# Kernel optimization log

Measured on AMD Instinct MI355X. Metric: run time of the kernel, lower is better.

Reference implementation:

```python
import jax, jax.numpy as jnp
import numpy as np

N_NODES = 100000
N_EDGES = 1600000
D = 64


def setup_inputs() -> dict:
    key = jax.random.key(0)
    k1, k2, k3, k4 = jax.random.split(key, 4)
    x = jax.random.normal(k1, (N_NODES, D), dtype=jnp.float32)
    src = jax.random.randint(k2, (N_EDGES,), 0, N_NODES, dtype=jnp.int64)
    dst = jax.random.randint(k3, (N_EDGES,), 0, N_NODES, dtype=jnp.int64)
    W = jax.random.normal(k4, (D, D), dtype=jnp.float32) / np.sqrt(D)
    b = jnp.zeros((D,), dtype=jnp.float32)
    return {"x": x, "src": src, "dst": dst, "W": W, "b": b}


def reference(x, src, dst, W, b):
    # DGL GraphConv, norm='both': h = D_in^{-1/2} A D_out^{-1/2} x W + b
    n = x.shape[0]
    ones = jnp.ones(src.shape[0], dtype=x.dtype)
    deg_out = jax.ops.segment_sum(ones, src, num_segments=n)  # out-degree of sources
    deg_in = jax.ops.segment_sum(ones, dst, num_segments=n)   # in-degree of dests
    norm_src = jnp.maximum(deg_out, 1.0) ** -0.5              # DGL clamps degs to >=1
    norm_dst = jnp.maximum(deg_in, 1.0) ** -0.5
    x_n = x * norm_src[:, None]                               # [N, D]
    agg = jax.ops.segment_sum(x_n[src], dst, num_segments=n)  # SpMM: [N, D]
    h = agg * norm_dst[:, None]
    # linear transform + bias; activation=None, dropout=0.0 (identity)
    return h @ W + b
```

## Files before the change

kernel.cpp:

```cpp
#include <hip/hip_runtime.h>
#include <hip/hip_bf16.h>

#define ND 64

#define DBKT_W 64
#define LOG_DBKT 6
#define NDBKT_MAX 1600
#define DCAP 1280

#define SBKT_W 256
#define LOG_SBKT 8
#define NSBKT_MAX 400
#define SCAP 4608

#define PART_EDGES 6400
#define COL_CAP DCAP

typedef __attribute__((ext_vector_type(8))) short bf16x8;
typedef __attribute__((ext_vector_type(4))) float f32x4;

__device__ __forceinline__ unsigned bf16rn(float f) {
    unsigned u = __float_as_uint(f);
    return (u + 0x7fffu + ((u >> 16) & 1u)) >> 16;
}
__device__ __forceinline__ unsigned pack2(float lo, float hi) {
    return bf16rn(lo) | (bf16rn(hi) << 16);
}

__global__ __launch_bounds__(256) void part_kernel(
        const int* __restrict__ src, const int* __restrict__ dst,
        int* __restrict__ cnt_d, int* __restrict__ cnt_s,
        int* __restrict__ ebuf, unsigned char* __restrict__ ebuf2,
        int E, int nbkt_d, int nbkt_s) {
    __shared__ int hbd[NDBKT_MAX], hcd[NDBKT_MAX];
    __shared__ int hbs[NSBKT_MAX], hcs[NSBKT_MAX];
    const int base_e = blockIdx.x * PART_EDGES;
    const int nE = min(PART_EDGES, E - base_e);
    for (int i = threadIdx.x; i < nbkt_d; i += blockDim.x) { hbd[i] = 0; hcd[i] = 0; }
    for (int i = threadIdx.x; i < nbkt_s; i += blockDim.x) { hbs[i] = 0; hcs[i] = 0; }
    __syncthreads();
    const int nq = nE >> 2;
    for (int i = threadIdx.x; i < nq; i += blockDim.x) {
        int4 s = ((const int4*)(src + base_e))[i];
        int4 d = ((const int4*)(dst + base_e))[i];
        atomicAdd(&hbd[d.x >> LOG_DBKT], 1); atomicAdd(&hbd[d.y >> LOG_DBKT], 1);
        atomicAdd(&hbd[d.z >> LOG_DBKT], 1); atomicAdd(&hbd[d.w >> LOG_DBKT], 1);
        atomicAdd(&hbs[s.x >> LOG_SBKT], 1); atomicAdd(&hbs[s.y >> LOG_SBKT], 1);
        atomicAdd(&hbs[s.z >> LOG_SBKT], 1); atomicAdd(&hbs[s.w >> LOG_SBKT], 1);
    }
    for (int e = (nq << 2) + threadIdx.x; e < nE; e += blockDim.x) {
        atomicAdd(&hbd[dst[base_e + e] >> LOG_DBKT], 1);
        atomicAdd(&hbs[src[base_e + e] >> LOG_SBKT], 1);
    }
    __syncthreads();
    for (int i = threadIdx.x; i < nbkt_d; i += blockDim.x) {
        int c = hbd[i];
        hbd[i] = c ? (i * DCAP + atomicAdd(&cnt_d[i], c)) : 0;
    }
    for (int i = threadIdx.x; i < nbkt_s; i += blockDim.x) {
        int c = hbs[i];
        hbs[i] = c ? (i * SCAP + atomicAdd(&cnt_s[i], c)) : 0;
    }
    __syncthreads();
    for (int i = threadIdx.x; i < nq; i += blockDim.x) {
        int4 s = ((const int4*)(src + base_e))[i];
        int4 d = ((const int4*)(dst + base_e))[i];
        int b0 = d.x >> LOG_DBKT, b1 = d.y >> LOG_DBKT;
        int b2 = d.z >> LOG_DBKT, b3 = d.w >> LOG_DBKT;
        int p0 = hbd[b0] + atomicAdd(&hcd[b0], 1);
        int p1 = hbd[b1] + atomicAdd(&hcd[b1], 1);
        int p2 = hbd[b2] + atomicAdd(&hcd[b2], 1);
        int p3 = hbd[b3] + atomicAdd(&hcd[b3], 1);
        if (p0 < (b0 + 1) * DCAP) ebuf[p0] = (s.x << LOG_DBKT) | (d.x & (DBKT_W - 1));
        if (p1 < (b1 + 1) * DCAP) ebuf[p1] = (s.y << LOG_DBKT) | (d.y & (DBKT_W - 1));
        if (p2 < (b2 + 1) * DCAP) ebuf[p2] = (s.z << LOG_DBKT) | (d.z & (DBKT_W - 1));
        if (p3 < (b3 + 1) * DCAP) ebuf[p3] = (s.w << LOG_DBKT) | (d.w & (DBKT_W - 1));
        int c0 = s.x >> LOG_SBKT, c1 = s.y >> LOG_SBKT;
        int c2 = s.z >> LOG_SBKT, c3 = s.w >> LOG_SBKT;
        int q0 = hbs[c0] + atomicAdd(&hcs[c0], 1);
        int q1 = hbs[c1] + atomicAdd(&hcs[c1], 1);
        int q2 = hbs[c2] + atomicAdd(&hcs[c2], 1);
        int q3 = hbs[c3] + atomicAdd(&hcs[c3], 1);
        if (q0 < (c0 + 1) * SCAP) ebuf2[q0] = (unsigned char)(s.x & (SBKT_W - 1));
        if (q1 < (c1 + 1) * SCAP) ebuf2[q1] = (unsigned char)(s.y & (SBKT_W - 1));
        if (q2 < (c2 + 1) * SCAP) ebuf2[q2] = (unsigned char)(s.z & (SBKT_W - 1));
        if (q3 < (c3 + 1) * SCAP) ebuf2[q3] = (unsigned char)(s.w & (SBKT_W - 1));
    }
    for (int e = (nq << 2) + threadIdx.x; e < nE; e += blockDim.x) {
        int s = src[base_e + e], d = dst[base_e + e];
        int bk = d >> LOG_DBKT;
        int p = hbd[bk] + atomicAdd(&hcd[bk], 1);
        if (p < (bk + 1) * DCAP) ebuf[p] = (s << LOG_DBKT) | (d & (DBKT_W - 1));
        int ck = s >> LOG_SBKT;
        int q = hbs[ck] + atomicAdd(&hcs[ck], 1);
        if (q < (ck + 1) * SCAP) ebuf2[q] = (unsigned char)(s & (SBKT_W - 1));
    }
}

__global__ __launch_bounds__(256) void yprep_kernel(
        const float4* __restrict__ x4,
        const unsigned char* __restrict__ ebuf2,
        const int* __restrict__ cnt_s,
        uint4* __restrict__ y4,
        const float* __restrict__ W, unsigned* __restrict__ wpk, int n) {
    __shared__ int cnt[SBKT_W];
    const int bkt = blockIdx.x;
    const int node0 = bkt << LOG_SBKT;
    if (threadIdx.x < SBKT_W) cnt[threadIdx.x] = 0;
    if (bkt == 0) {
        for (int i = threadIdx.x; i < 2048; i += blockDim.x) {
            int l = i >> 5, d = i & 31;
            int colb = l & 15, kb = (l >> 4) * 8;
            int t = d >> 3, s = (d >> 2) & 1, m = d & 3;
            float lo = W[(32 * s + kb + 2 * m) * ND + 16 * t + colb];
            float hi = W[(32 * s + kb + 2 * m + 1) * ND + 16 * t + colb];
            wpk[i] = pack2(lo, hi);
        }
    }
    __syncthreads();
    const int beg = bkt * SCAP;
    const int end = beg + min(cnt_s[bkt], SCAP);
    for (int i = beg + (int)threadIdx.x; i < end; i += blockDim.x)
        atomicAdd(&cnt[ebuf2[i]], 1);
    __syncthreads();
#pragma unroll
    for (int it = 0; it < 8; ++it) {
        int item = it * 256 + threadIdx.x;
        int row = item >> 3, q = item & 7;
        int grow = node0 + row;
        if (grow >= n) continue;
        float nr = rsqrtf(fmaxf((float)cnt[row], 1.0f));
        float4 a = x4[(size_t)grow * 16 + q * 2];
        float4 b = x4[(size_t)grow * 16 + q * 2 + 1];
        uint4 o;
        o.x = pack2(a.x * nr, a.y * nr);
        o.y = pack2(a.z * nr, a.w * nr);
        o.z = pack2(b.x * nr, b.y * nr);
        o.w = pack2(b.z * nr, b.w * nr);
        y4[(size_t)grow * 8 + q] = o;
    }
}

__global__ __launch_bounds__(256) void spmm_kernel(
        const unsigned* __restrict__ y32,
        const int* __restrict__ ebuf,
        const int* __restrict__ cnt_d,
        const unsigned* __restrict__ wpk,
        const float* __restrict__ bias,
        float* __restrict__ out, int n, int nbkt) {
    __shared__ int colS[COL_CAP];
    __shared__ int rp[DBKT_W + 1];
    __shared__ int cur[DBKT_W];
    __shared__ int degl[DBKT_W];
    __shared__ unsigned hS[4][16 * 32];

    const int lane = threadIdx.x & 63;
    const int q    = lane >> 4;
    const int f    = lane & 15;
    const int g    = threadIdx.x >> 6;
    const int colb = lane & 15;
    const uint2* Y2 = (const uint2*)y32;

    bf16x8 bw[4][2];
#pragma unroll
    for (int t = 0; t < 4; ++t)
#pragma unroll
        for (int s = 0; s < 2; ++s)
            bw[t][s] = *(const bf16x8*)&wpk[lane * 32 + (t * 2 + s) * 4];
    float bb[4];
#pragma unroll
    for (int t = 0; t < 4; ++t) bb[t] = bias[16 * t + colb];

    for (int bkt = blockIdx.x; bkt < nbkt; bkt += gridDim.x) {
        const int ebeg = bkt * DCAP;
        const int ne   = min(cnt_d[bkt], DCAP);
        const int node0 = bkt << LOG_DBKT;
        const int nn = min(DBKT_W, n - node0);

        if (threadIdx.x < DBKT_W) degl[threadIdx.x] = 0;
        __syncthreads();
        for (int i = threadIdx.x; i < ne; i += blockDim.x)
            atomicAdd(&degl[ebuf[ebeg + i] & (DBKT_W - 1)], 1);
        __syncthreads();
        if (g == 0) {
            int v = degl[lane];
            int sv = v;
#pragma unroll
            for (int off = 1; off < 64; off <<= 1) {
                int t = __shfl_up(sv, off, 64);
                if (lane >= off) sv += t;
            }
            int ex = sv - v;
            rp[lane] = ex;
            cur[lane] = ex;
            if (lane == 63) rp[DBKT_W] = sv;
        }
        __syncthreads();
        for (int i = threadIdx.x; i < ne; i += blockDim.x) {
            int p = ebuf[ebeg + i];
            int pos = atomicAdd(&cur[p & (DBKT_W - 1)], 1);
            if (pos < COL_CAP) colS[pos] = p >> LOG_DBKT;
        }
        __syncthreads();

#pragma unroll 1
        for (int it = 0; it < 4; ++it) {
            const int ln = (g << 4) + (it << 2) + q;
            const bool act = ln < nn;
            const int beg = act ? rp[ln] : 0;
            const int end = act ? rp[ln + 1] : 0;
            float A0 = 0.f, A1 = 0.f, A2 = 0.f, A3 = 0.f;
            float B0 = 0.f, B1 = 0.f, B2 = 0.f, B3 = 0.f;
            int j = beg;
            for (; j + 8 <= end; j += 8) {
                int e0 = colS[j],     e1 = colS[j + 1];
                int e2 = colS[j + 2], e3 = colS[j + 3];
                int e4 = colS[j + 4], e5 = colS[j + 5];
                int e6 = colS[j + 6], e7 = colS[j + 7];
                uint2 u0 = Y2[(size_t)e0 * 16 + f];
                uint2 u1 = Y2[(size_t)e1 * 16 + f];
                uint2 u2 = Y2[(size_t)e2 * 16 + f];
                uint2 u3 = Y2[(size_t)e3 * 16 + f];
                uint2 u4 = Y2[(size_t)e4 * 16 + f];
                uint2 u5 = Y2[(size_t)e5 * 16 + f];
                uint2 u6 = Y2[(size_t)e6 * 16 + f];
                uint2 u7 = Y2[(size_t)e7 * 16 + f];
                A0 += __uint_as_float(u0.x << 16); A1 += __uint_as_float(u0.x & 0xffff0000u);
                A2 += __uint_as_float(u0.y << 16); A3 += __uint_as_float(u0.y & 0xffff0000u);
                B0 += __uint_as_float(u1.x << 16); B1 += __uint_as_float(u1.x & 0xffff0000u);
                B2 += __uint_as_float(u1.y << 16); B3 += __uint_as_float(u1.y & 0xffff0000u);
                A0 += __uint_as_float(u2.x << 16); A1 += __uint_as_float(u2.x & 0xffff0000u);
                A2 += __uint_as_float(u2.y << 16); A3 += __uint_as_float(u2.y & 0xffff0000u);
                B0 += __uint_as_float(u3.x << 16); B1 += __uint_as_float(u3.x & 0xffff0000u);
                B2 += __uint_as_float(u3.y << 16); B3 += __uint_as_float(u3.y & 0xffff0000u);
                A0 += __uint_as_float(u4.x << 16); A1 += __uint_as_float(u4.x & 0xffff0000u);
                A2 += __uint_as_float(u4.y << 16); A3 += __uint_as_float(u4.y & 0xffff0000u);
                B0 += __uint_as_float(u5.x << 16); B1 += __uint_as_float(u5.x & 0xffff0000u);
                B2 += __uint_as_float(u5.y << 16); B3 += __uint_as_float(u5.y & 0xffff0000u);
                A0 += __uint_as_float(u6.x << 16); A1 += __uint_as_float(u6.x & 0xffff0000u);
                A2 += __uint_as_float(u6.y << 16); A3 += __uint_as_float(u6.y & 0xffff0000u);
                B0 += __uint_as_float(u7.x << 16); B1 += __uint_as_float(u7.x & 0xffff0000u);
                B2 += __uint_as_float(u7.y << 16); B3 += __uint_as_float(u7.y & 0xffff0000u);
            }
            for (; j + 2 <= end; j += 2) {
                int e0 = colS[j], e1 = colS[j + 1];
                uint2 u0 = Y2[(size_t)e0 * 16 + f];
                uint2 u1 = Y2[(size_t)e1 * 16 + f];
                A0 += __uint_as_float(u0.x << 16); A1 += __uint_as_float(u0.x & 0xffff0000u);
                A2 += __uint_as_float(u0.y << 16); A3 += __uint_as_float(u0.y & 0xffff0000u);
                B0 += __uint_as_float(u1.x << 16); B1 += __uint_as_float(u1.x & 0xffff0000u);
                B2 += __uint_as_float(u1.y << 16); B3 += __uint_as_float(u1.y & 0xffff0000u);
            }
            if (j < end) {
                int e0 = colS[j];
                uint2 u0 = Y2[(size_t)e0 * 16 + f];
                A0 += __uint_as_float(u0.x << 16); A1 += __uint_as_float(u0.x & 0xffff0000u);
                A2 += __uint_as_float(u0.y << 16); A3 += __uint_as_float(u0.y & 0xffff0000u);
            }
            if (act) {
                float nd = rsqrtf(fmaxf((float)(end - beg), 1.0f));
                uint2 wv;
                wv.x = pack2((A0 + B0) * nd, (A1 + B1) * nd);
                wv.y = pack2((A2 + B2) * nd, (A3 + B3) * nd);
                *(uint2*)&hS[g][(((it << 2) + q) << 5) + (f << 1)] = wv;
            }
        }
        __syncthreads();

        if ((g << 4) < nn) {
            const unsigned* hrow = &hS[g][colb * 32 + ((lane >> 4) << 2)];
            bf16x8 a0 = *(const bf16x8*)hrow;
            bf16x8 a1 = *(const bf16x8*)(hrow + 16);
#pragma unroll
            for (int t = 0; t < 4; ++t) {
                f32x4 z = {0.f, 0.f, 0.f, 0.f};
                z = __builtin_amdgcn_mfma_f32_16x16x32_bf16(a0, bw[t][0], z, 0, 0, 0);
                z = __builtin_amdgcn_mfma_f32_16x16x32_bf16(a1, bw[t][1], z, 0, 0, 0);
#pragma unroll
                for (int r = 0; r < 4; ++r) {
                    int rowD = ((lane >> 4) << 2) + r;
                    int li = (g << 4) + rowD;
                    if (li < nn)
                        out[(size_t)(node0 + li) * ND + 16 * t + colb] = z[r] + bb[t];
                }
            }
        }
        __syncthreads();
    }
}

extern "C" void kernel_launch(void* const* d_in, const int* in_sizes, int n_in,
                              void* d_out, int out_size, void* d_ws, size_t ws_size,
                              hipStream_t stream) {
    const float* x   = (const float*)d_in[0];
    const int*   src = (const int*)d_in[1];
    const int*   dst = (const int*)d_in[2];
    const float* W   = (const float*)d_in[3];
    const float* b   = (const float*)d_in[4];
    float*       out = (float*)d_out;

    const int n = in_sizes[0] / ND;
    const int E = in_sizes[1];
    const int nbkt_d = (n + DBKT_W - 1) / DBKT_W;
    const int nbkt_s = (n + SBKT_W - 1) / SBKT_W;

    char* ws = (char*)d_ws;
    unsigned* y32   = (unsigned*)ws;
    int*      ebuf  = (int*)(y32 + (size_t)n * 32);
    int*      cnt_d = ebuf + (size_t)NDBKT_MAX * DCAP;
    int*      cnt_s = cnt_d + NDBKT_MAX;
    unsigned* wpk   = (unsigned*)(cnt_s + NSBKT_MAX);
    unsigned char* ebuf2 = (unsigned char*)(wpk + 2048);

    hipMemsetAsync(cnt_d, 0, (size_t)(NDBKT_MAX + NSBKT_MAX) * sizeof(int), stream);

    part_kernel<<<(E + PART_EDGES - 1) / PART_EDGES, 256, 0, stream>>>(
        src, dst, cnt_d, cnt_s, ebuf, ebuf2, E, nbkt_d, nbkt_s);
    yprep_kernel<<<nbkt_s, 256, 0, stream>>>(
        (const float4*)x, ebuf2, cnt_s, (uint4*)y32, W, wpk, n);
    spmm_kernel<<<nbkt_d, 256, 0, stream>>>(y32, ebuf, cnt_d, wpk, b, out, n, nbkt_d);
}
```

Before: 99.57 us.

## Widen SpMM gathers to 16-byte rows, shrink partition blocks, register-cache edges

The partition kernel now takes 2048 edges per block. Each thread holds its 8 edges in registers, and the base offsets are bumped in place, which removes the second counter arrays and the second global read. The degree-count kernel reads the byte bucket 16 bytes at a time. The SpMM kernel caches bucket edges in registers between the degree pass and the scatter pass. It also gathers 16-byte rows with 8 lanes per node instead of 8-byte rows with 16 lanes, so more nodes are in flight per wave at the cost of more registers. The fast partition path relies on the 2048-edge block size exactly matching 2 int4 loads per thread.

Measured after the change: 118.5 us. 1.19x slower.

```diff
diff --git a/kernel.cpp b/kernel.cpp
--- a/kernel.cpp
+++ b/kernel.cpp
@@ -13,7 +13,7 @@
 #define NSBKT_MAX 400
 #define SCAP 4608
 
-#define PART_EDGES 6400
+#define PART_EDGES 2048
 #define COL_CAP DCAP
 
 typedef __attribute__((ext_vector_type(8))) short bf16x8;
@@ -32,68 +32,76 @@
         int* __restrict__ cnt_d, int* __restrict__ cnt_s,
         int* __restrict__ ebuf, unsigned char* __restrict__ ebuf2,
         int E, int nbkt_d, int nbkt_s) {
-    __shared__ int hbd[NDBKT_MAX], hcd[NDBKT_MAX];
-    __shared__ int hbs[NSBKT_MAX], hcs[NSBKT_MAX];
+    __shared__ int hbd[NDBKT_MAX];
+    __shared__ int hbs[NSBKT_MAX];
     const int base_e = blockIdx.x * PART_EDGES;
     const int nE = min(PART_EDGES, E - base_e);
-    for (int i = threadIdx.x; i < nbkt_d; i += blockDim.x) { hbd[i] = 0; hcd[i] = 0; }
-    for (int i = threadIdx.x; i < nbkt_s; i += blockDim.x) { hbs[i] = 0; hcs[i] = 0; }
+    for (int i = threadIdx.x; i < nbkt_d; i += blockDim.x) hbd[i] = 0;
+    for (int i = threadIdx.x; i < nbkt_s; i += blockDim.x) hbs[i] = 0;
     __syncthreads();
-    const int nq = nE >> 2;
-    for (int i = threadIdx.x; i < nq; i += blockDim.x) {
-        int4 s = ((const int4*)(src + base_e))[i];
-        int4 d = ((const int4*)(dst + base_e))[i];
-        atomicAdd(&hbd[d.x >> LOG_DBKT], 1); atomicAdd(&hbd[d.y >> LOG_DBKT], 1);
-        atomicAdd(&hbd[d.z >> LOG_DBKT], 1); atomicAdd(&hbd[d.w >> LOG_DBKT], 1);
-        atomicAdd(&hbs[s.x >> LOG_SBKT], 1); atomicAdd(&hbs[s.y >> LOG_SBKT], 1);
-        atomicAdd(&hbs[s.z >> LOG_SBKT], 1); atomicAdd(&hbs[s.w >> LOG_SBKT], 1);
-    }
-    for (int e = (nq << 2) + threadIdx.x; e < nE; e += blockDim.x) {
-        atomicAdd(&hbd[dst[base_e + e] >> LOG_DBKT], 1);
-        atomicAdd(&hbs[src[base_e + e] >> LOG_SBKT], 1);
-    }
-    __syncthreads();
-    for (int i = threadIdx.x; i < nbkt_d; i += blockDim.x) {
-        int c = hbd[i];
-        hbd[i] = c ? (i * DCAP + atomicAdd(&cnt_d[i], c)) : 0;
-    }
-    for (int i = threadIdx.x; i < nbkt_s; i += blockDim.x) {
-        int c = hbs[i];
-        hbs[i] = c ? (i * SCAP + atomicAdd(&cnt_s[i], c)) : 0;
-    }
-    __syncthreads();
-    for (int i = threadIdx.x; i < nq; i += blockDim.x) {
-        int4 s = ((const int4*)(src + base_e))[i];
-        int4 d = ((const int4*)(dst + base_e))[i];
-        int b0 = d.x >> LOG_DBKT, b1 = d.y >> LOG_DBKT;
-        int b2 = d.z >> LOG_DBKT, b3 = d.w >> LOG_DBKT;
-        int p0 = hbd[b0] + atomicAdd(&hcd[b0], 1);
-        int p1 = hbd[b1] + atomicAdd(&hcd[b1], 1);
-        int p2 = hbd[b2] + atomicAdd(&hcd[b2], 1);
-        int p3 = hbd[b3] + atomicAdd(&hcd[b3], 1);
-        if (p0 < (b0 + 1) * DCAP) ebuf[p0] = (s.x << LOG_DBKT) | (d.x & (DBKT_W - 1));
-        if (p1 < (b1 + 1) * DCAP) ebuf[p1] = (s.y << LOG_DBKT) | (d.y & (DBKT_W - 1));
-        if (p2 < (b2 + 1) * DCAP) ebuf[p2] = (s.z << LOG_DBKT) | (d.z & (DBKT_W - 1));
-        if (p3 < (b3 + 1) * DCAP) ebuf[p3] = (s.w << LOG_DBKT) | (d.w & (DBKT_W - 1));
-        int c0 = s.x >> LOG_SBKT, c1 = s.y >> LOG_SBKT;
-        int c2 = s.z >> LOG_SBKT, c3 = s.w >> LOG_SBKT;
-        int q0 = hbs[c0] + atomicAdd(&hcs[c0], 1);
-        int q1 = hbs[c1] + atomicAdd(&hcs[c1], 1);
-        int q2 = hbs[c2] + atomicAdd(&hcs[c2], 1);
-        int q3 = hbs[c3] + atomicAdd(&hcs[c3], 1);
-        if (q0 < (c0 + 1) * SCAP) ebuf2[q0] = (unsigned char)(s.x & (SBKT_W - 1));
-        if (q1 < (c1 + 1) * SCAP) ebuf2[q1] = (unsigned char)(s.y & (SBKT_W - 1));
-        if (q2 < (c2 + 1) * SCAP) ebuf2[q2] = (unsigned char)(s.z & (SBKT_W - 1));
-        if (q3 < (c3 + 1) * SCAP) ebuf2[q3] = (unsigned char)(s.w & (SBKT_W - 1));
-    }
-    for (int e = (nq << 2) + threadIdx.x; e < nE; e += blockDim.x) {
-        int s = src[base_e + e], d = dst[base_e + e];
-        int bk = d >> LOG_DBKT;
-        int p = hbd[bk] + atomicAdd(&hcd[bk], 1);
-        if (p < (bk + 1) * DCAP) ebuf[p] = (s << LOG_DBKT) | (d & (DBKT_W - 1));
-        int ck = s >> LOG_SBKT;
-        int q = hbs[ck] + atomicAdd(&hcs[ck], 1);
-        if (q < (ck + 1) * SCAP) ebuf2[q] = (unsigned char)(s & (SBKT_W - 1));
+
+    if (nE == PART_EDGES) {
+        const int4* s4 = (const int4*)(src + base_e);
+        const int4* d4 = (const int4*)(dst + base_e);
+        int4 s0 = s4[threadIdx.x], s1 = s4[256 + threadIdx.x];
+        int4 d0 = d4[threadIdx.x], d1 = d4[256 + threadIdx.x];
+        atomicAdd(&hbd[d0.x >> LOG_DBKT], 1); atomicAdd(&hbd[d0.y >> LOG_DBKT], 1);
+        atomicAdd(&hbd[d0.z >> LOG_DBKT], 1); atomicAdd(&hbd[d0.w >> LOG_DBKT], 1);
+        atomicAdd(&hbd[d1.x >> LOG_DBKT], 1); atomicAdd(&hbd[d1.y >> LOG_DBKT], 1);
+        atomicAdd(&hbd[d1.z >> LOG_DBKT], 1); atomicAdd(&hbd[d1.w >> LOG_DBKT], 1);
+        atomicAdd(&hbs[s0.x >> LOG_SBKT], 1); atomicAdd(&hbs[s0.y >> LOG_SBKT], 1);
+        atomicAdd(&hbs[s0.z >> LOG_SBKT], 1); atomicAdd(&hbs[s0.w >> LOG_SBKT], 1);
+        atomicAdd(&hbs[s1.x >> LOG_SBKT], 1); atomicAdd(&hbs[s1.y >> LOG_SBKT], 1);
+        atomicAdd(&hbs[s1.z >> LOG_SBKT], 1); atomicAdd(&hbs[s1.w >> LOG_SBKT], 1);
+        __syncthreads();
+        for (int i = threadIdx.x; i < nbkt_d; i += blockDim.x) {
+            int c = hbd[i];
+            hbd[i] = c ? (i * DCAP + atomicAdd(&cnt_d[i], c)) : 0;
+        }
+        for (int i = threadIdx.x; i < nbkt_s; i += blockDim.x) {
+            int c = hbs[i];
+            hbs[i] = c ? (i * SCAP + atomicAdd(&cnt_s[i], c)) : 0;
+        }
+        __syncthreads();
+        {
+            int sv[8] = {s0.x, s0.y, s0.z, s0.w, s1.x, s1.y, s1.z, s1.w};
+            int dv[8] = {d0.x, d0.y, d0.z, d0.w, d1.x, d1.y, d1.z, d1.w};
+#pragma unroll
+            for (int k = 0; k < 8; ++k) {
+                int b = dv[k] >> LOG_DBKT;
+                int p = atomicAdd(&hbd[b], 1);
+                if (p < (b + 1) * DCAP)
+                    ebuf[p] = (sv[k] << LOG_DBKT) | (dv[k] & (DBKT_W - 1));
+                int c = sv[k] >> LOG_SBKT;
+                int q = atomicAdd(&hbs[c], 1);
+                if (q < (c + 1) * SCAP)
+                    ebuf2[q] = (unsigned char)(sv[k] & (SBKT_W - 1));
+            }
+        }
+    } else {
+        for (int e = (int)threadIdx.x; e < nE; e += blockDim.x) {
+            atomicAdd(&hbd[dst[base_e + e] >> LOG_DBKT], 1);
+            atomicAdd(&hbs[src[base_e + e] >> LOG_SBKT], 1);
+        }
+        __syncthreads();
+        for (int i = threadIdx.x; i < nbkt_d; i += blockDim.x) {
+            int c = hbd[i];
+            hbd[i] = c ? (i * DCAP + atomicAdd(&cnt_d[i], c)) : 0;
+        }
+        for (int i = threadIdx.x; i < nbkt_s; i += blockDim.x) {
+            int c = hbs[i];
+            hbs[i] = c ? (i * SCAP + atomicAdd(&cnt_s[i], c)) : 0;
+        }
+        __syncthreads();
+        for (int e = (int)threadIdx.x; e < nE; e += blockDim.x) {
+            int s = src[base_e + e], d = dst[base_e + e];
+            int b = d >> LOG_DBKT;
+            int p = atomicAdd(&hbd[b], 1);
+            if (p < (b + 1) * DCAP) ebuf[p] = (s << LOG_DBKT) | (d & (DBKT_W - 1));
+            int c = s >> LOG_SBKT;
+            int q = atomicAdd(&hbs[c], 1);
+            if (q < (c + 1) * SCAP) ebuf2[q] = (unsigned char)(s & (SBKT_W - 1));
+        }
     }
 }
 
@@ -118,10 +126,22 @@
         }
     }
     __syncthreads();
-    const int beg = bkt * SCAP;
-    const int end = beg + min(cnt_s[bkt], SCAP);
-    for (int i = beg + (int)threadIdx.x; i < end; i += blockDim.x)
-        atomicAdd(&cnt[ebuf2[i]], 1);
+    const int ce = min(cnt_s[bkt], SCAP);
+    const uint4* b16 = (const uint4*)(ebuf2 + (size_t)bkt * SCAP);
+    const int nq = ce >> 4;
+    for (int i = threadIdx.x; i < nq; i += blockDim.x) {
+        uint4 v = b16[i];
+#pragma unroll
+        for (int w = 0; w < 4; ++w) {
+            unsigned u = (&v.x)[w];
+            atomicAdd(&cnt[u & 255], 1);
+            atomicAdd(&cnt[(u >> 8) & 255], 1);
+            atomicAdd(&cnt[(u >> 16) & 255], 1);
+            atomicAdd(&cnt[u >> 24], 1);
+        }
+    }
+    for (int i = (nq << 4) + (int)threadIdx.x; i < ce; i += blockDim.x)
+        atomicAdd(&cnt[ebuf2[(size_t)bkt * SCAP + i]], 1);
     __syncthreads();
 #pragma unroll
     for (int it = 0; it < 8; ++it) {
@@ -154,12 +174,12 @@
     __shared__ int degl[DBKT_W];
     __shared__ unsigned hS[4][16 * 32];
 
-    const int lane = threadIdx.x & 63;
-    const int q    = lane >> 4;
-    const int f    = lane & 15;
-    const int g    = threadIdx.x >> 6;
-    const int colb = lane & 15;
-    const uint2* Y2 = (const uint2*)y32;
+    const int lane  = threadIdx.x & 63;
+    const int chain = lane >> 3;
+    const int r     = lane & 7;
+    const int g     = threadIdx.x >> 6;
+    const int colb  = lane & 15;
+    const uint4* Y4 = (const uint4*)y32;
 
     bf16x8 bw[4][2];
 #pragma unroll
@@ -179,8 +199,13 @@
 
         if (threadIdx.x < DBKT_W) degl[threadIdx.x] = 0;
         __syncthreads();
-        for (int i = threadIdx.x; i < ne; i += blockDim.x)
-            atomicAdd(&degl[ebuf[ebeg + i] & (DBKT_W - 1)], 1);
+        int ev[5];
+#pragma unroll
+        for (int k = 0; k < 5; ++k) {
+            int i = (int)threadIdx.x + (k << 8);
+            ev[k] = (i < ne) ? ebuf[ebeg + i] : -1;
+            if (ev[k] >= 0) atomicAdd(&degl[ev[k] & (DBKT_W - 1)], 1);
+        }
         __syncthreads();
         if (g == 0) {
             int v = degl[lane];
@@ -196,73 +221,64 @@
             if (lane == 63) rp[DBKT_W] = sv;
         }
         __syncthreads();
-        for (int i = threadIdx.x; i < ne; i += blockDim.x) {
-            int p = ebuf[ebeg + i];
-            int pos = atomicAdd(&cur[p & (DBKT_W - 1)], 1);
-            if (pos < COL_CAP) colS[pos] = p >> LOG_DBKT;
+#pragma unroll
+        for (int k = 0; k < 5; ++k) {
+            if (ev[k] >= 0) {
+                int pos = atomicAdd(&cur[ev[k] & (DBKT_W - 1)], 1);
+                if (pos < COL_CAP) colS[pos] = ev[k] >> LOG_DBKT;
+            }
         }
         __syncthreads();
 
 #pragma unroll 1
-        for (int it = 0; it < 4; ++it) {
-            const int ln = (g << 4) + (it << 2) + q;
+        for (int it = 0; it < 2; ++it) {
+            const int ln = (g << 4) + (it << 3) + chain;
             const bool act = ln < nn;
             const int beg = act ? rp[ln] : 0;
             const int end = act ? rp[ln + 1] : 0;
             float A0 = 0.f, A1 = 0.f, A2 = 0.f, A3 = 0.f;
-            float B0 = 0.f, B1 = 0.f, B2 = 0.f, B3 = 0.f;
+            float A4 = 0.f, A5 = 0.f, A6 = 0.f, A7 = 0.f;
             int j = beg;
             for (; j + 8 <= end; j += 8) {
                 int e0 = colS[j],     e1 = colS[j + 1];
                 int e2 = colS[j + 2], e3 = colS[j + 3];
                 int e4 = colS[j + 4], e5 = colS[j + 5];
                 int e6 = colS[j + 6], e7 = colS[j + 7];
-                uint2 u0 = Y2[(size_t)e0 * 16 + f];
-                uint2 u1 = Y2[(size_t)e1 * 16 + f];
-                uint2 u2 = Y2[(size_t)e2 * 16 + f];
-                uint2 u3 = Y2[(size_t)e3 * 16 + f];
-                uint2 u4 = Y2[(size_t)e4 * 16 + f];
-                uint2 u5 = Y2[(size_t)e5 * 16 + f];
-                uint2 u6 = Y2[(size_t)e6 * 16 + f];
-                uint2 u7 = Y2[(size_t)e7 * 16 + f];
-                A0 += __uint_as_float(u0.x << 16); A1 += __uint_as_float(u0.x & 0xffff0000u);
-                A2 += __uint_as_float(u0.y << 16); A3 += __uint_as_float(u0.y & 0xffff0000u);
-                B0 += __uint_as_float(u1.x << 16); B1 += __uint_as_float(u1.x & 0xffff0000u);
-                B2 += __uint_as_float(u1.y << 16); B3 += __uint_as_float(u1.y & 0xffff0000u);
-                A0 += __uint_as_float(u2.x << 16); A1 += __uint_as_float(u2.x & 0xffff0000u);
-                A2 += __uint_as_float(u2.y << 16); A3 += __uint_as_float(u2.y & 0xffff0000u);
-                B0 += __uint_as_float(u3.x << 16); B1 += __uint_as_float(u3.x & 0xffff0000u);
-                B2 += __uint_as_float(u3.y << 16); B3 += __uint_as_float(u3.y & 0xffff0000u);
-                A0 += __uint_as_float(u4.x << 16); A1 += __uint_as_float(u4.x & 0xffff0000u);
-                A2 += __uint_as_float(u4.y << 16); A3 += __uint_as_float(u4.y & 0xffff0000u);
-                B0 += __uint_as_float(u5.x << 16); B1 += __uint_as_float(u5.x & 0xffff0000u);
-                B2 += __uint_as_float(u5.y << 16); B3 += __uint_as_float(u5.y & 0xffff0000u);
-                A0 += __uint_as_float(u6.x << 16); A1 += __uint_as_float(u6.x & 0xffff0000u);
-                A2 += __uint_as_float(u6.y << 16); A3 += __uint_as_float(u6.y & 0xffff0000u);
-                B0 += __uint_as_float(u7.x << 16); B1 += __uint_as_float(u7.x & 0xffff0000u);
-                B2 += __uint_as_float(u7.y << 16); B3 += __uint_as_float(u7.y & 0xffff0000u);
+                uint4 u0 = Y4[(size_t)e0 * 8 + r];
+                uint4 u1 = Y4[(size_t)e1 * 8 + r];
+                uint4 u2 = Y4[(size_t)e2 * 8 + r];
+                uint4 u3 = Y4[(size_t)e3 * 8 + r];
+                uint4 u4 = Y4[(size_t)e4 * 8 + r];
+                uint4 u5 = Y4[(size_t)e5 * 8 + r];
+                uint4 u6 = Y4[(size_t)e6 * 8 + r];
+                uint4 u7 = Y4[(size_t)e7 * 8 + r];
+#define ACC(u) \
+                A0 += __uint_as_float((u).x << 16); A1 += __uint_as_float((u).x & 0xffff0000u); \
+                A2 += __uint_as_float((u).y << 16); A3 += __uint_as_float((u).y & 0xffff0000u); \
+                A4 += __uint_as_float((u).z << 16); A5 += __uint_as_float((u).z & 0xffff0000u); \
+                A6 += __uint_as_float((u).w << 16); A7 += __uint_as_float((u).w & 0xffff0000u);
+                ACC(u0) ACC(u1) ACC(u2) ACC(u3) ACC(u4) ACC(u5) ACC(u6) ACC(u7)
             }
             for (; j + 2 <= end; j += 2) {
                 int e0 = colS[j], e1 = colS[j + 1];
-                uint2 u0 = Y2[(size_t)e0 * 16 + f];
-                uint2 u1 = Y2[(size_t)e1 * 16 + f];
-                A0 += __uint_as_float(u0.x << 16); A1 += __uint_as_float(u0.x & 0xffff0000u);
-                A2 += __uint_as_float(u0.y << 16); A3 += __uint_as_float(u0.y & 0xffff0000u);
-                B0 += __uint_as_float(u1.x << 16); B1 += __uint_as_float(u1.x & 0xffff0000u);
-                B2 += __uint_as_float(u1.y << 16); B3 += __uint_as_float(u1.y & 0xffff0000u);
+                uint4 u0 = Y4[(size_t)e0 * 8 + r];
+                uint4 u1 = Y4[(size_t)e1 * 8 + r];
+                ACC(u0) ACC(u1)
             }
             if (j < end) {
-                int e0 = colS[j];
-                uint2 u0 = Y2[(size_t)e0 * 16 + f];
-                A0 += __uint_as_float(u0.x << 16); A1 += __uint_as_float(u0.x & 0xffff0000u);
-                A2 += __uint_as_float(u0.y << 16); A3 += __uint_as_float(u0.y & 0xffff0000u);
-            }
+                uint4 u0 = Y4[(size_t)colS[j] * 8 + r];
+                ACC(u0)
+            }
+#undef ACC
             if (act) {
                 float nd = rsqrtf(fmaxf((float)(end - beg), 1.0f));
-                uint2 wv;
-                wv.x = pack2((A0 + B0) * nd, (A1 + B1) * nd);
-                wv.y = pack2((A2 + B2) * nd, (A3 + B3) * nd);
-                *(uint2*)&hS[g][(((it << 2) + q) << 5) + (f << 1)] = wv;
+                uint4 wv;
+                wv.x = pack2(A0 * nd, A1 * nd);
+                wv.y = pack2(A2 * nd, A3 * nd);
+                wv.z = pack2(A4 * nd, A5 * nd);
+                wv.w = pack2(A6 * nd, A7 * nd);
+                const int idx = (it << 3) + chain;
+                *(uint4*)&hS[g][(idx << 5) + (r << 2)] = wv;
             }
         }
         __syncthreads();
@@ -277,11 +293,11 @@
                 z = __builtin_amdgcn_mfma_f32_16x16x32_bf16(a0, bw[t][0], z, 0, 0, 0);
                 z = __builtin_amdgcn_mfma_f32_16x16x32_bf16(a1, bw[t][1], z, 0, 0, 0);
 #pragma unroll
-                for (int r = 0; r < 4; ++r) {
-                    int rowD = ((lane >> 4) << 2) + r;
+                for (int rr = 0; rr < 4; ++rr) {
+                    int rowD = ((lane >> 4) << 2) + rr;
                     int li = (g << 4) + rowD;
                     if (li < nn)
-                        out[(size_t)(node0 + li) * ND + 16 * t + colb] = z[r] + bb[t];
+                        out[(size_t)(node0 + li) * ND + 16 * t + colb] = z[rr] + bb[t];
                 }
             }
         }
```
